# Performance work log

Measured on AMD Instinct MI355X. Metric: run time of the kernel, lower is better.

## Reference

```python
import jax, jax.numpy as jnp
import numpy as np

N_HEAD = 16

def setup_inputs() -> dict:
    key = jax.random.key(0)
    k0, k1, k2, k3, k4 = jax.random.split(key, 5)
    B, T, C = 4, 2048, 1024
    x = jax.random.normal(k0, (B, T, C), dtype=jnp.float32)
    # torch nn.Linear weights are (out_features, in_features); scale like kaiming-uniform-ish
    s = 1.0 / np.sqrt(C)
    Wk = jax.random.uniform(k1, (C, C), jnp.float32, -s, s)
    Wq = jax.random.uniform(k2, (C, C), jnp.float32, -s, s)
    Wv = jax.random.uniform(k3, (C, C), jnp.float32, -s, s)
    Wo = jax.random.uniform(k4, (C, C), jnp.float32, -s, s)
    return {"x": x, "Wk": Wk, "Wq": Wq, "Wv": Wv, "Wo": Wo}

def reference(x, Wk, Wq, Wv, Wo):
    B, T, C = x.shape
    hs = C // N_HEAD
    # projections (torch Linear: y = x @ W.T), split heads -> (B, nh, T, hs)
    def proj(W):
        return (x @ W.T).reshape(B, T, N_HEAD, hs).transpose(0, 2, 1, 3)
    k = proj(Wk)
    q = proj(Wq)
    v = proj(Wv)
    # dot attention: scale by sqrt(head_dim) (k.shape[2] after transpose in source)
    score = jnp.einsum('bhqd,bhkd->bhqk', q, k) / jnp.sqrt(jnp.asarray(hs, x.dtype))
    # NOTE: source calls score.masked_fill(mask, -inf) without assignment -> mask has no effect.
    e = jax.nn.softmax(score, axis=-1)
    o = jnp.einsum('bhqk,bhkd->bhqd', e, v)          # (B, nh, T, hs)
    o = o.transpose(0, 2, 1, 3).reshape(B, T, C)     # merge heads
    o = o @ Wo.T                                      # final projection
    # dropout is identity in eval mode
    return o
```

## Files before the change

kernel.cpp:

```cpp
#include <hip/hip_runtime.h>
#include <hip/hip_bf16.h>
#include <cstddef>
#include <cstdint>

#define B_DIM 4
#define T_DIM 2048
#define C_DIM 1024
#define NHEAD 16
#define HS    64
#define QKV_LD 3072

#define QSCALE 0.18033688011112042f

typedef __attribute__((ext_vector_type(8))) short short8;
typedef __attribute__((ext_vector_type(4))) float f32x4;

__device__ __forceinline__ short f2bf(float x) {
    __hip_bfloat16 b = __float2bfloat16(x);
    return *reinterpret_cast<short*>(&b);
}

__device__ __forceinline__ void load_lds16(const void* g, void* l) {
    __builtin_amdgcn_global_load_lds(
        (const __attribute__((address_space(1))) void*)(g),
        (__attribute__((address_space(3))) void*)(l),
        16, 0, 0);
}

__global__ __launch_bounds__(256) void cast_bf16(
    const float* __restrict__ in, short* __restrict__ out, int n8, float scale)
{
    int i = blockIdx.x * 256 + threadIdx.x;
    if (i >= n8) return;
    const float4* p = (const float4*)in + (size_t)i * 2;
    float4 a = p[0], b = p[1];
    short8 o;
    o[0]=f2bf(a.x*scale); o[1]=f2bf(a.y*scale); o[2]=f2bf(a.z*scale); o[3]=f2bf(a.w*scale);
    o[4]=f2bf(b.x*scale); o[5]=f2bf(b.y*scale); o[6]=f2bf(b.z*scale); o[7]=f2bf(b.w*scale);
    *((short8*)out + i) = o;
}

__global__ __launch_bounds__(256) void cast4_bf16(
    const float* __restrict__ w0, const float* __restrict__ w1,
    const float* __restrict__ w2, const float* __restrict__ w3,
    short* __restrict__ out, int n8)
{
    int i = blockIdx.x * 256 + threadIdx.x;
    if (i >= n8) return;
    const int sel = blockIdx.y;
    const float* in = (sel == 0) ? w0 : (sel == 1) ? w1 : (sel == 2) ? w2 : w3;
    const float scale = (sel == 0) ? QSCALE : 1.0f;
    const float4* p = (const float4*)in + (size_t)i * 2;
    float4 a = p[0], b = p[1];
    short8 o;
    o[0]=f2bf(a.x*scale); o[1]=f2bf(a.y*scale); o[2]=f2bf(a.z*scale); o[3]=f2bf(a.w*scale);
    o[4]=f2bf(b.x*scale); o[5]=f2bf(b.y*scale); o[6]=f2bf(b.z*scale); o[7]=f2bf(b.w*scale);
    *((short8*)out + (size_t)sel * n8 + i) = o;
}

__global__ __launch_bounds__(512, 2) void gemm_bt_8ph(
    const short* __restrict__ A,
    const short* __restrict__ Bm,
    short* __restrict__ Cm,
    int M, int N, int K)
{
    __shared__ __align__(16) short lds[65536];

    const int nbx = N >> 8;
    int wg = blockIdx.x;
    const int cpx = gridDim.x >> 3;
    wg = (wg & 7) * cpx + (wg >> 3);
    const int bx = wg % nbx, by = wg / nbx;
    const int m0 = by << 8, n0 = bx << 8;

    const int t = threadIdx.x;
    const int w = t >> 6, lane = t & 63;
    const int l16 = lane & 15, quad = lane >> 4;
    const int wm = w >> 2, wn = w & 3;

    const int rcall  = t >> 3;
    const int chunk  = t & 7;
    const int schunk = chunk ^ (rcall & 7);
    const int dstrow = w * 8;

    const short* AgT = A  + (size_t)(m0 + rcall) * K + schunk * 8;
    const short* AgB = AgT + (size_t)128 * K;
    const short* BgT = Bm + (size_t)(n0 + rcall) * K + schunk * 8;
    const short* BgB = BgT + (size_t)128 * K;

    int aoff[8][2], boff[4][2];
    #pragma unroll
    for (int mf = 0; mf < 8; ++mf) {
        const int ar = wm * 128 + mf * 16 + l16;
        #pragma unroll
        for (int ks = 0; ks < 2; ++ks)
            aoff[mf][ks] = ar * 64 + (((ks * 4 + quad) ^ (ar & 7)) * 8);
    }
    #pragma unroll
    for (int nf = 0; nf < 4; ++nf) {
        const int br = wn * 64 + nf * 16 + l16;
        #pragma unroll
        for (int ks = 0; ks < 2; ++ks)
            boff[nf][ks] = br * 64 + (((ks * 4 + quad) ^ (br & 7)) * 8);
    }

    f32x4 acc[8][4];
    const f32x4 zero4 = {0.f, 0.f, 0.f, 0.f};
    #pragma unroll
    for (int mf = 0; mf < 8; ++mf)
        #pragma unroll
        for (int nf = 0; nf < 4; ++nf) acc[mf][nf] = zero4;

    const int NT = K >> 6;

    #define STAGE_HALF(gbase, kt, lhalf)                                        \
        {                                                                        \
            load_lds16((gbase) + (size_t)(kt) * 64,                              \
                       (lhalf) + dstrow * 64);                                   \
            load_lds16((gbase) + (size_t)64 * K + (size_t)(kt) * 64,             \
                       (lhalf) + (64 + dstrow) * 64);                            \
        }

    STAGE_HALF(AgT, 0, lds);
    STAGE_HALF(AgB, 0, lds + 128 * 64);
    STAGE_HALF(BgT, 0, lds + 32768);
    STAGE_HALF(BgB, 0, lds + 32768 + 128 * 64);
    STAGE_HALF(AgT, 1, lds + 16384);

    for (int kt = 0; kt < NT; ++kt) {
        const int b0 = kt & 1;
        const short* Acur = lds + b0 * 16384;
        const short* Bcur = lds + 32768 + b0 * 16384;
        short* Anx = lds + (b0 ^ 1) * 16384;
        short* Bnx = lds + 32768 + (b0 ^ 1) * 16384;

        if (kt == NT - 1) asm volatile("s_waitcnt vmcnt(0)" ::: "memory");
        else              asm volatile("s_waitcnt vmcnt(2)" ::: "memory");
        __builtin_amdgcn_s_barrier();

        short8 bfr[4][2];
        #pragma unroll
        for (int nf = 0; nf < 4; ++nf)
            #pragma unroll
            for (int ks = 0; ks < 2; ++ks)
                bfr[nf][ks] = *(const short8*)(Bcur + boff[nf][ks]);

        #pragma unroll
        for (int ph = 0; ph < 4; ++ph) {
            short8 af[2][2];
            #pragma unroll
            for (int r = 0; r < 2; ++r)
                #pragma unroll
                for (int ks = 0; ks < 2; ++ks)
                    af[r][ks] = *(const short8*)(Acur + aoff[ph * 2 + r][ks]);

            if (ph == 0)      { if (kt + 1 < NT) STAGE_HALF(AgB, kt + 1, Anx + 128 * 64); }
            else if (ph == 1) { if (kt + 1 < NT) STAGE_HALF(BgT, kt + 1, Bnx); }
            else if (ph == 2) { if (kt + 1 < NT) STAGE_HALF(BgB, kt + 1, Bnx + 128 * 64); }

            __builtin_amdgcn_s_barrier();
            __builtin_amdgcn_s_setprio(1);
            #pragma unroll
            for (int r = 0; r < 2; ++r)
                #pragma unroll
                for (int nf = 0; nf < 4; ++nf)
                    #pragma unroll
                    for (int ks = 0; ks < 2; ++ks)
                        acc[ph * 2 + r][nf] = __builtin_amdgcn_mfma_f32_16x16x32_bf16(
                            af[r][ks], bfr[nf][ks], acc[ph * 2 + r][nf], 0, 0, 0);
            __builtin_amdgcn_s_setprio(0);
            __builtin_amdgcn_s_barrier();
        }

        if (kt + 2 < NT) { short* Aw = lds + b0 * 16384; STAGE_HALF(AgT, kt + 2, Aw); }
    }
    #undef STAGE_HALF

    #pragma unroll
    for (int mf = 0; mf < 8; ++mf) {
        const int row_base = m0 + wm * 128 + mf * 16 + quad * 4;
        #pragma unroll
        for (int nf = 0; nf < 4; ++nf) {
            const int col = n0 + wn * 64 + nf * 16 + l16;
            #pragma unroll
            for (int r = 0; r < 4; ++r)
                Cm[(size_t)(row_base + r) * N + col] = f2bf(acc[mf][nf][r]);
        }
    }
}

#define BM 128
#define BN 128
#define BK 32

template<bool OUT_BF16>
__global__ __launch_bounds__(256) void gemm_bt_mfma(
    const short* __restrict__ A,
    const short* __restrict__ Bm,
    void* __restrict__ Cm,
    int M, int N, int K, float scale)
{
    __shared__ __align__(16) short smem[8192];
    short* As = smem;
    short* Bs = smem + 4096;

    const int m0 = blockIdx.y * BM;
    const int n0 = blockIdx.x * BN;
    const int t    = threadIdx.x;
    const int w    = t >> 6;
    const int lane = t & 63;
    const int l16  = lane & 15;
    const int quad = lane >> 4;
    const int wm   = w >> 1;
    const int wn   = w & 1;

    const int mS0 = t >> 2;
    const int qS  = (t & 3) ^ ((t >> 3) & 3);
    const short* aG0 = A  + (size_t)(m0 + mS0)      * K + qS * 8;
    const short* aG1 = A  + (size_t)(m0 + mS0 + 64) * K + qS * 8;
    const short* bG0 = Bm + (size_t)(n0 + mS0)      * K + qS * 8;
    const short* bG1 = Bm + (size_t)(n0 + mS0 + 64) * K + qS * 8;
    short* aL0 = As + (size_t)(w * 64) * 8;
    short* aL1 = As + (size_t)(256 + w * 64) * 8;
    short* bL0 = Bs + (size_t)(w * 64) * 8;
    short* bL1 = Bs + (size_t)(256 + w * 64) * 8;

    int a_off[4], b_off[4];
    #pragma unroll
    for (int i = 0; i < 4; ++i) {
        int am = wm * 64 + i * 16 + l16;
        a_off[i] = (am * 4 + (quad ^ ((am >> 1) & 3))) * 8;
        int bn = wn * 64 + i * 16 + l16;
        b_off[i] = (bn * 4 + (quad ^ ((bn >> 1) & 3))) * 8;
    }

    f32x4 acc[4][4];
    const f32x4 zero4 = {0.f, 0.f, 0.f, 0.f};
    #pragma unroll
    for (int i = 0; i < 4; ++i)
        #pragma unroll
        for (int j = 0; j < 4; ++j) acc[i][j] = zero4;

    for (int k0 = 0; k0 < K; k0 += BK) {
        __syncthreads();
        load_lds16(aG0 + k0, aL0);
        load_lds16(aG1 + k0, aL1);
        load_lds16(bG0 + k0, bL0);
        load_lds16(bG1 + k0, bL1);
        __syncthreads();

        short8 af[4], bf[4];
        #pragma unroll
        for (int i = 0; i < 4; ++i) {
            af[i] = *(const short8*)(As + a_off[i]);
            bf[i] = *(const short8*)(Bs + b_off[i]);
        }
        #pragma unroll
        for (int i = 0; i < 4; ++i)
            #pragma unroll
            for (int j = 0; j < 4; ++j)
                acc[i][j] = __builtin_amdgcn_mfma_f32_16x16x32_bf16(
                    af[i], bf[j], acc[i][j], 0, 0, 0);
    }

    #pragma unroll
    for (int i = 0; i < 4; ++i) {
        const int row_base = m0 + wm * 64 + i * 16 + quad * 4;
        #pragma unroll
        for (int j = 0; j < 4; ++j) {
            const int col = n0 + wn * 64 + j * 16 + l16;
            #pragma unroll
            for (int r = 0; r < 4; ++r) {
                const size_t idx = (size_t)(row_base + r) * N + col;
                if (OUT_BF16) ((short*)Cm)[idx] = f2bf(acc[i][j][r] * scale);
                else          ((float*)Cm)[idx] = acc[i][j][r] * scale;
            }
        }
    }
}

__global__ __launch_bounds__(256) void transpose_v(
    const short* __restrict__ Vb,
    short* __restrict__ Vt, int srcLD)
{
    const int t0 = blockIdx.x * 64;
    const int head = blockIdx.y;
    const int b = head >> 4, h = head & 15;

    __shared__ short Ls[64][72];

    const int t = threadIdx.x;
    const int r = t >> 2;
    const int c = (t & 3) * 16;

    const short* src = Vb + ((size_t)(b * T_DIM) + t0 + r) * srcLD + h * HS + c;
    *(short8*)&Ls[r][c]     = *(const short8*)src;
    *(short8*)&Ls[r][c + 8] = *(const short8*)(src + 8);
    __syncthreads();

    short tmp[16];
    #pragma unroll
    for (int i = 0; i < 16; ++i) tmp[i] = Ls[c + i][r];
    short* dst = Vt + ((size_t)head * HS + r) * T_DIM + t0 + c;
    *(short8*)dst       = *(short8*)&tmp[0];
    *(short8*)(dst + 8) = *(short8*)&tmp[8];
}

#define QSUB 4

__global__ __launch_bounds__(256, 2) void attn_mfma3(
    const short* __restrict__ Qb,
    const short* __restrict__ Kb,
    const short* __restrict__ Vt,
    short* __restrict__ O)
{
    const int i0   = blockIdx.x * (64 * QSUB);
    const int head = blockIdx.y;
    const int b = head >> 4, h = head & 15;

    const int t    = threadIdx.x;
    const int w    = t >> 6;
    const int lane = t & 63;
    const int l16  = lane & 15;
    const int quad = lane >> 4;

    __shared__ __align__(16) short Ks[64][64];
    __shared__ __align__(16) short Vts[64][64];

    short8 qf[QSUB][2];
    #pragma unroll
    for (int sub = 0; sub < QSUB; ++sub) {
        const short* qrow = Qb
            + ((size_t)(b * T_DIM) + i0 + sub * 64 + w * 16 + l16) * QKV_LD + h * HS;
        qf[sub][0] = *(const short8*)(qrow + quad * 8);
        qf[sub][1] = *(const short8*)(qrow + 32 + quad * 8);
    }

    short8 onesv;
    #pragma unroll
    for (int j = 0; j < 8; ++j) onesv[j] = (short)0x3F80;

    const f32x4 zero4 = {0.f, 0.f, 0.f, 0.f};
    f32x4 oacc[QSUB][4];
    f32x4 lacc[QSUB];
    #pragma unroll
    for (int sub = 0; sub < QSUB; ++sub) {
        #pragma unroll
        for (int dg = 0; dg < 4; ++dg) oacc[sub][dg] = zero4;
        lacc[sub] = zero4;
    }

    const int sr  = t >> 2;
    const int sc2 = (t & 3) * 2;
    const int krow = (sr & 32) | ((sr & 4) << 2) | ((sr & 24) >> 1) | (sr & 3);
    const short* kgbase = Kb + (size_t)(b * T_DIM) * QKV_LD + h * HS;
    const short* vgbase = Vt + ((size_t)head * HS + sr) * T_DIM;

    short* kd0 = &Ks[krow][((sc2    ) ^ (krow & 7)) * 8];
    short* kd1 = &Ks[krow][((sc2 + 1) ^ (krow & 7)) * 8];
    short* vd0 = &Vts[sr][((sc2    ) ^ (sr & 7)) * 8];
    short* vd1 = &Vts[sr][((sc2 + 1) ^ (sr & 7)) * 8];

    const int x7 = l16 & 7;

    for (int j0 = 0; j0 < T_DIM; j0 += 64) {
        __syncthreads();
        {
            const short* kp = kgbase + (size_t)(j0 + sr) * QKV_LD + sc2 * 8;
            *(short8*)kd0 = *(const short8*)kp;
            *(short8*)kd1 = *(const short8*)(kp + 8);
            const short* vp = vgbase + j0 + sc2 * 8;
            *(short8*)vd0 = *(const short8*)vp;
            *(short8*)vd1 = *(const short8*)(vp + 8);
        }
        __syncthreads();

        short8 ka[4][2], va[4][2];
        #pragma unroll
        for (int kt = 0; kt < 4; ++kt) {
            const int row = kt * 16 + l16;
            ka[kt][0] = *(const short8*)&Ks[row][((quad    ) ^ x7) * 8];
            ka[kt][1] = *(const short8*)&Ks[row][((quad + 4) ^ x7) * 8];
            va[kt][0] = *(const short8*)&Vts[row][((quad    ) ^ x7) * 8];
            va[kt][1] = *(const short8*)&Vts[row][((quad + 4) ^ x7) * 8];
        }

        #pragma unroll
        for (int sub = 0; sub < QSUB; ++sub) {
            f32x4 s[4];
            #pragma unroll
            for (int kt = 0; kt < 4; ++kt) {
                f32x4 acc = zero4;
                acc = __builtin_amdgcn_mfma_f32_16x16x32_bf16(ka[kt][0], qf[sub][0], acc, 0, 0, 0);
                acc = __builtin_amdgcn_mfma_f32_16x16x32_bf16(ka[kt][1], qf[sub][1], acc, 0, 0, 0);
                s[kt] = acc;
            }

            short8 pa[2];
            #pragma unroll
            for (int hh = 0; hh < 2; ++hh) {
                #pragma unroll
                for (int c = 0; c < 2; ++c) {
                    f32x4 sv = s[2 * hh + c];
                    #pragma unroll
                    for (int r = 0; r < 4; ++r) {
                        float p = __builtin_amdgcn_exp2f(sv[r]);
                        pa[hh][c * 4 + r] = f2bf(p);
                    }
                }
            }

            lacc[sub] = __builtin_amdgcn_mfma_f32_16x16x32_bf16(pa[0], onesv, lacc[sub], 0, 0, 0);
            lacc[sub] = __builtin_amdgcn_mfma_f32_16x16x32_bf16(pa[1], onesv, lacc[sub], 0, 0, 0);

            #pragma unroll
            for (int dg = 0; dg < 4; ++dg) {
                oacc[sub][dg] = __builtin_amdgcn_mfma_f32_16x16x32_bf16(pa[0], va[dg][0], oacc[sub][dg], 0, 0, 0);
                oacc[sub][dg] = __builtin_amdgcn_mfma_f32_16x16x32_bf16(pa[1], va[dg][1], oacc[sub][dg], 0, 0, 0);
            }
        }
    }

    #pragma unroll
    for (int sub = 0; sub < QSUB; ++sub) {
        float linv[4];
        #pragma unroll
        for (int r = 0; r < 4; ++r) linv[r] = 1.0f / lacc[sub][r];

        #pragma unroll
        for (int r = 0; r < 4; ++r) {
            short* orow = O + ((size_t)(b * T_DIM) + i0 + sub * 64 + w * 16 + quad * 4 + r) * C_DIM + h * HS;
            #pragma unroll
            for (int dg = 0; dg < 4; ++dg)
                orow[dg * 16 + l16] = f2bf(oacc[sub][dg][r] * linv[r]);
        }
    }
}

extern "C" void kernel_launch(void* const* d_in, const int* in_sizes, int n_in,
                              void* d_out, int out_size, void* d_ws, size_t ws_size,
                              hipStream_t stream) {
    const float* x  = (const float*)d_in[0];
    const float* Wk = (const float*)d_in[1];
    const float* Wq = (const float*)d_in[2];
    const float* Wv = (const float*)d_in[3];
    const float* Wo = (const float*)d_in[4];
    float* out = (float*)d_out;

    const int M = B_DIM * T_DIM;
    const size_t NE = (size_t)M * C_DIM;
    const size_t NB = 2 * NE;
    const size_t WB = (size_t)2 * C_DIM * C_DIM;
    const size_t WE = (size_t)C_DIM * C_DIM;

    char* ws = (char*)d_ws;
    short* xb   = (short*)(ws);
    short* Ob   = xb;
    short* QKVb = (short*)(ws + NB);
    short* Vtb  = (short*)(ws + 4 * NB);
    short* W3b  = (short*)(ws + 5 * NB);
    short* Wob  = (short*)(ws + 5 * NB + 3 * WB);

    cast_bf16<<<(int)(NE / 8 / 256), 256, 0, stream>>>(x, xb, (int)(NE / 8), 1.0f);
    const int wn8 = (int)(WE / 8);
    cast4_bf16<<<dim3(wn8 / 256, 4), 256, 0, stream>>>(Wq, Wk, Wv, Wo, W3b, wn8);

    gemm_bt_8ph<<<dim3((QKV_LD / 256) * (M / 256)), 512, 0, stream>>>(
        xb, W3b, QKVb, M, QKV_LD, C_DIM);

    transpose_v<<<dim3(T_DIM / 64, B_DIM * NHEAD), 256, 0, stream>>>(
        QKVb + 2 * C_DIM, Vtb, QKV_LD);

    attn_mfma3<<<dim3(T_DIM / (64 * QSUB), B_DIM * NHEAD), 256, 0, stream>>>(
        QKVb, QKVb + C_DIM, Vtb, Ob);

    gemm_bt_mfma<false><<<dim3(C_DIM / BN, M / BM), 256, 0, stream>>>(
        Ob, Wob, out, M, C_DIM, C_DIM, 1.0f);
}
```

Measured before the change: 262.6 us.

## Shrink 8-phase GEMM tile to 128x256 and reuse it for output projection

The pipelined bf16 GEMM kernel now uses a 128x256 tile instead of 256x256, with two compute phases per k-step and smaller LDS, and gains a template flag for fp32 output. The QKV projection launches twice as many workgroups, and the output projection switches from the simple 128x128 single-buffered GEMM to this pipelined kernel. The intent is better CU fill on the 256-CU device and overlapped, double-buffered loads for the final projection, at the cost of less data reuse per tile in the QKV GEMM.

```diff
diff --git a/kernel.cpp b/kernel.cpp
--- a/kernel.cpp
+++ b/kernel.cpp
@@ -58,20 +58,21 @@
     *((short8*)out + (size_t)sel * n8 + i) = o;
 }
 
+template<bool OUT_BF16>
 __global__ __launch_bounds__(512, 2) void gemm_bt_8ph(
     const short* __restrict__ A,
     const short* __restrict__ Bm,
-    short* __restrict__ Cm,
+    void* __restrict__ Cm,
     int M, int N, int K)
 {
-    __shared__ __align__(16) short lds[65536];
+    __shared__ __align__(16) short lds[49152];
 
     const int nbx = N >> 8;
     int wg = blockIdx.x;
     const int cpx = gridDim.x >> 3;
     wg = (wg & 7) * cpx + (wg >> 3);
     const int bx = wg % nbx, by = wg / nbx;
-    const int m0 = by << 8, n0 = bx << 8;
+    const int m0 = by << 7, n0 = bx << 8;
 
     const int t = threadIdx.x;
     const int w = t >> 6, lane = t & 63;
@@ -79,19 +80,21 @@
     const int wm = w >> 2, wn = w & 3;
 
     const int rcall  = t >> 3;
-    const int chunk  = t & 7;
-    const int schunk = chunk ^ (rcall & 7);
-    const int dstrow = w * 8;
-
-    const short* AgT = A  + (size_t)(m0 + rcall) * K + schunk * 8;
-    const short* AgB = AgT + (size_t)128 * K;
-    const short* BgT = Bm + (size_t)(n0 + rcall) * K + schunk * 8;
-    const short* BgB = BgT + (size_t)128 * K;
-
-    int aoff[8][2], boff[4][2];
-    #pragma unroll
-    for (int mf = 0; mf < 8; ++mf) {
-        const int ar = wm * 128 + mf * 16 + l16;
+    const int schunk = (t & 7) ^ (rcall & 7);
+    const int dstoff = w * 512;
+
+    const short* Ag = A  + (size_t)(m0 + rcall) * K + schunk * 8;
+    const short* Bg = Bm + (size_t)(n0 + rcall) * K + schunk * 8;
+
+    short* const Ab0 = lds;
+    short* const Ab1 = lds + 8192;
+    short* const Bb0 = lds + 16384;
+    short* const Bb1 = lds + 32768;
+
+    int aoff[4][2], boff[4][2];
+    #pragma unroll
+    for (int mf = 0; mf < 4; ++mf) {
+        const int ar = wm * 64 + mf * 16 + l16;
         #pragma unroll
         for (int ks = 0; ks < 2; ++ks)
             aoff[mf][ks] = ar * 64 + (((ks * 4 + quad) ^ (ar & 7)) * 8);
@@ -104,176 +107,100 @@
             boff[nf][ks] = br * 64 + (((ks * 4 + quad) ^ (br & 7)) * 8);
     }
 
-    f32x4 acc[8][4];
+    f32x4 acc[4][4];
     const f32x4 zero4 = {0.f, 0.f, 0.f, 0.f};
     #pragma unroll
-    for (int mf = 0; mf < 8; ++mf)
+    for (int mf = 0; mf < 4; ++mf)
         #pragma unroll
         for (int nf = 0; nf < 4; ++nf) acc[mf][nf] = zero4;
 
     const int NT = K >> 6;
 
-    #define STAGE_HALF(gbase, kt, lhalf)                                        \
-        {                                                                        \
-            load_lds16((gbase) + (size_t)(kt) * 64,                              \
-                       (lhalf) + dstrow * 64);                                   \
-            load_lds16((gbase) + (size_t)64 * K + (size_t)(kt) * 64,             \
-                       (lhalf) + (64 + dstrow) * 64);                            \
-        }
-
-    STAGE_HALF(AgT, 0, lds);
-    STAGE_HALF(AgB, 0, lds + 128 * 64);
-    STAGE_HALF(BgT, 0, lds + 32768);
-    STAGE_HALF(BgB, 0, lds + 32768 + 128 * 64);
-    STAGE_HALF(AgT, 1, lds + 16384);
+    #define ST64(gb, kt, ro, lb)                                               \
+        load_lds16((gb) + (size_t)(ro) * K + (size_t)(kt) * 64,                \
+                   (lb) + (ro) * 64 + dstoff)
+
+    ST64(Ag, 0, 0, Ab0); ST64(Ag, 0, 64, Ab0);
+    ST64(Bg, 0, 0, Bb0); ST64(Bg, 0, 64, Bb0);
+    ST64(Bg, 0, 128, Bb0); ST64(Bg, 0, 192, Bb0);
+    ST64(Ag, 1, 0, Ab1); ST64(Ag, 1, 64, Ab1);
 
     for (int kt = 0; kt < NT; ++kt) {
-        const int b0 = kt & 1;
-        const short* Acur = lds + b0 * 16384;
-        const short* Bcur = lds + 32768 + b0 * 16384;
-        short* Anx = lds + (b0 ^ 1) * 16384;
-        short* Bnx = lds + 32768 + (b0 ^ 1) * 16384;
+        short* Acur = (kt & 1) ? Ab1 : Ab0;
+        short* Bcur = (kt & 1) ? Bb1 : Bb0;
+        short* Bnx  = (kt & 1) ? Bb0 : Bb1;
 
         if (kt == NT - 1) asm volatile("s_waitcnt vmcnt(0)" ::: "memory");
         else              asm volatile("s_waitcnt vmcnt(2)" ::: "memory");
         __builtin_amdgcn_s_barrier();
 
-        short8 bfr[4][2];
+        short8 bfr[4][2], af[2][2];
         #pragma unroll
         for (int nf = 0; nf < 4; ++nf)
             #pragma unroll
             for (int ks = 0; ks < 2; ++ks)
                 bfr[nf][ks] = *(const short8*)(Bcur + boff[nf][ks]);
-
-        #pragma unroll
-        for (int ph = 0; ph < 4; ++ph) {
-            short8 af[2][2];
-            #pragma unroll
-            for (int r = 0; r < 2; ++r)
+        #pragma unroll
+        for (int mf = 0; mf < 2; ++mf)
+            #pragma unroll
+            for (int ks = 0; ks < 2; ++ks)
+                af[mf][ks] = *(const short8*)(Acur + aoff[mf][ks]);
+
+        if (kt + 1 < NT) { ST64(Bg, kt + 1, 0, Bnx); ST64(Bg, kt + 1, 64, Bnx); }
+
+        __builtin_amdgcn_s_barrier();
+        __builtin_amdgcn_s_setprio(1);
+        #pragma unroll
+        for (int mf = 0; mf < 2; ++mf)
+            #pragma unroll
+            for (int nf = 0; nf < 4; ++nf)
                 #pragma unroll
                 for (int ks = 0; ks < 2; ++ks)
-                    af[r][ks] = *(const short8*)(Acur + aoff[ph * 2 + r][ks]);
-
-            if (ph == 0)      { if (kt + 1 < NT) STAGE_HALF(AgB, kt + 1, Anx + 128 * 64); }
-            else if (ph == 1) { if (kt + 1 < NT) STAGE_HALF(BgT, kt + 1, Bnx); }
-            else if (ph == 2) { if (kt + 1 < NT) STAGE_HALF(BgB, kt + 1, Bnx + 128 * 64); }
-
-            __builtin_amdgcn_s_barrier();
-            __builtin_amdgcn_s_setprio(1);
-            #pragma unroll
-            for (int r = 0; r < 2; ++r)
+                    acc[mf][nf] = __builtin_amdgcn_mfma_f32_16x16x32_bf16(
+                        af[mf][ks], bfr[nf][ks], acc[mf][nf], 0, 0, 0);
+        __builtin_amdgcn_s_setprio(0);
+        __builtin_amdgcn_s_barrier();
+
+        short8 af2[2][2];
+        #pragma unroll
+        for (int mf = 0; mf < 2; ++mf)
+            #pragma unroll
+            for (int ks = 0; ks < 2; ++ks)
+                af2[mf][ks] = *(const short8*)(Acur + aoff[2 + mf][ks]);
+
+        if (kt + 1 < NT) { ST64(Bg, kt + 1, 128, Bnx); ST64(Bg, kt + 1, 192, Bnx); }
+
+        __builtin_amdgcn_s_barrier();
+        __builtin_amdgcn_s_setprio(1);
+        #pragma unroll
+        for (int mf = 0; mf < 2; ++mf)
+            #pragma unroll
+            for (int nf = 0; nf < 4; ++nf)
                 #pragma unroll
-                for (int nf = 0; nf < 4; ++nf)
-                    #pragma unroll
-                    for (int ks = 0; ks < 2; ++ks)
-                        acc[ph * 2 + r][nf] = __builtin_amdgcn_mfma_f32_16x16x32_bf16(
-                            af[r][ks], bfr[nf][ks], acc[ph * 2 + r][nf], 0, 0, 0);
-            __builtin_amdgcn_s_setprio(0);
-            __builtin_amdgcn_s_barrier();
-        }
-
-        if (kt + 2 < NT) { short* Aw = lds + b0 * 16384; STAGE_HALF(AgT, kt + 2, Aw); }
-    }
-    #undef STAGE_HALF
-
-    #pragma unroll
-    for (int mf = 0; mf < 8; ++mf) {
-        const int row_base = m0 + wm * 128 + mf * 16 + quad * 4;
+                for (int ks = 0; ks < 2; ++ks)
+                    acc[2 + mf][nf] = __builtin_amdgcn_mfma_f32_16x16x32_bf16(
+                        af2[mf][ks], bfr[nf][ks], acc[2 + mf][nf], 0, 0, 0);
+        __builtin_amdgcn_s_setprio(0);
+        __builtin_amdgcn_s_barrier();
+
+        if (kt + 2 < NT) {
+            short* Aw = (kt & 1) ? Ab1 : Ab0;
+            ST64(Ag, kt + 2, 0, Aw); ST64(Ag, kt + 2, 64, Aw);
+        }
+    }
+    #undef ST64
+
+    #pragma unroll
+    for (int mf = 0; mf < 4; ++mf) {
+        const int row_base = m0 + wm * 64 + mf * 16 + quad * 4;
         #pragma unroll
         for (int nf = 0; nf < 4; ++nf) {
             const int col = n0 + wn * 64 + nf * 16 + l16;
             #pragma unroll
-            for (int r = 0; r < 4; ++r)
-                Cm[(size_t)(row_base + r) * N + col] = f2bf(acc[mf][nf][r]);
-        }
-    }
-}
-
-#define BM 128
-#define BN 128
-#define BK 32
-
-template<bool OUT_BF16>
-__global__ __launch_bounds__(256) void gemm_bt_mfma(
-    const short* __restrict__ A,
-    const short* __restrict__ Bm,
-    void* __restrict__ Cm,
-    int M, int N, int K, float scale)
-{
-    __shared__ __align__(16) short smem[8192];
-    short* As = smem;
-    short* Bs = smem + 4096;
-
-    const int m0 = blockIdx.y * BM;
-    const int n0 = blockIdx.x * BN;
-    const int t    = threadIdx.x;
-    const int w    = t >> 6;
-    const int lane = t & 63;
-    const int l16  = lane & 15;
-    const int quad = lane >> 4;
-    const int wm   = w >> 1;
-    const int wn   = w & 1;
-
-    const int mS0 = t >> 2;
-    const int qS  = (t & 3) ^ ((t >> 3) & 3);
-    const short* aG0 = A  + (size_t)(m0 + mS0)      * K + qS * 8;
-    const short* aG1 = A  + (size_t)(m0 + mS0 + 64) * K + qS * 8;
-    const short* bG0 = Bm + (size_t)(n0 + mS0)      * K + qS * 8;
-    const short* bG1 = Bm + (size_t)(n0 + mS0 + 64) * K + qS * 8;
-    short* aL0 = As + (size_t)(w * 64) * 8;
-    short* aL1 = As + (size_t)(256 + w * 64) * 8;
-    short* bL0 = Bs + (size_t)(w * 64) * 8;
-    short* bL1 = Bs + (size_t)(256 + w * 64) * 8;
-
-    int a_off[4], b_off[4];
-    #pragma unroll
-    for (int i = 0; i < 4; ++i) {
-        int am = wm * 64 + i * 16 + l16;
-        a_off[i] = (am * 4 + (quad ^ ((am >> 1) & 3))) * 8;
-        int bn = wn * 64 + i * 16 + l16;
-        b_off[i] = (bn * 4 + (quad ^ ((bn >> 1) & 3))) * 8;
-    }
-
-    f32x4 acc[4][4];
-    const f32x4 zero4 = {0.f, 0.f, 0.f, 0.f};
-    #pragma unroll
-    for (int i = 0; i < 4; ++i)
-        #pragma unroll
-        for (int j = 0; j < 4; ++j) acc[i][j] = zero4;
-
-    for (int k0 = 0; k0 < K; k0 += BK) {
-        __syncthreads();
-        load_lds16(aG0 + k0, aL0);
-        load_lds16(aG1 + k0, aL1);
-        load_lds16(bG0 + k0, bL0);
-        load_lds16(bG1 + k0, bL1);
-        __syncthreads();
-
-        short8 af[4], bf[4];
-        #pragma unroll
-        for (int i = 0; i < 4; ++i) {
-            af[i] = *(const short8*)(As + a_off[i]);
-            bf[i] = *(const short8*)(Bs + b_off[i]);
-        }
-        #pragma unroll
-        for (int i = 0; i < 4; ++i)
-            #pragma unroll
-            for (int j = 0; j < 4; ++j)
-                acc[i][j] = __builtin_amdgcn_mfma_f32_16x16x32_bf16(
-                    af[i], bf[j], acc[i][j], 0, 0, 0);
-    }
-
-    #pragma unroll
-    for (int i = 0; i < 4; ++i) {
-        const int row_base = m0 + wm * 64 + i * 16 + quad * 4;
-        #pragma unroll
-        for (int j = 0; j < 4; ++j) {
-            const int col = n0 + wn * 64 + j * 16 + l16;
-            #pragma unroll
             for (int r = 0; r < 4; ++r) {
                 const size_t idx = (size_t)(row_base + r) * N + col;
-                if (OUT_BF16) ((short*)Cm)[idx] = f2bf(acc[i][j][r] * scale);
-                else          ((float*)Cm)[idx] = acc[i][j][r] * scale;
+                if (OUT_BF16) ((short*)Cm)[idx] = f2bf(acc[mf][nf][r]);
+                else          ((float*)Cm)[idx] = acc[mf][nf][r];
             }
         }
     }
@@ -465,7 +392,7 @@
     const int wn8 = (int)(WE / 8);
     cast4_bf16<<<dim3(wn8 / 256, 4), 256, 0, stream>>>(Wq, Wk, Wv, Wo, W3b, wn8);
 
-    gemm_bt_8ph<<<dim3((QKV_LD / 256) * (M / 256)), 512, 0, stream>>>(
+    gemm_bt_8ph<true><<<dim3((QKV_LD / 256) * (M / 128)), 512, 0, stream>>>(
         xb, W3b, QKVb, M, QKV_LD, C_DIM);
 
     transpose_v<<<dim3(T_DIM / 64, B_DIM * NHEAD), 256, 0, stream>>>(
@@ -474,6 +401,6 @@
     attn_mfma3<<<dim3(T_DIM / (64 * QSUB), B_DIM * NHEAD), 256, 0, stream>>>(
         QKVb, QKVb + C_DIM, Vtb, Ob);
 
-    gemm_bt_mfma<false><<<dim3(C_DIM / BN, M / BM), 256, 0, stream>>>(
-        Ob, Wob, out, M, C_DIM, C_DIM, 1.0f);
-}
+    gemm_bt_8ph<false><<<dim3((C_DIM / 256) * (M / 128)), 512, 0, stream>>>(
+        Ob, Wob, out, M, C_DIM, C_DIM);
+}
```

Measured after the change: 253.5 us. -3.5%, faster.
